# Kernel tuning notes

Measured on AMD Instinct MI355X. Metric: run time of the kernel, lower is better.

Reference implementation:

```python
import jax, jax.numpy as jnp
import numpy as np

B, DIN, DOUT, E = 131072, 512, 512, 16


def setup_inputs() -> dict:
    key = jax.random.key(0)
    k_x, k_wg, k_we = jax.random.split(key, 3)
    x = jax.random.normal(k_x, (B, DIN), dtype=jnp.float32)
    # gating network params
    Wg = jax.random.normal(k_wg, (DIN, E), dtype=jnp.float32) * 0.02
    bg = jnp.zeros((E,), dtype=jnp.float32)
    # GRN params (torch inits them to zero -> GRN is identity at init)
    gamma = jnp.zeros((E,), dtype=jnp.float32)
    beta = jnp.zeros((E,), dtype=jnp.float32)
    # per-expert linear params, stacked [E, DIN, DOUT]
    We = jax.random.normal(k_we, (E, DIN, DOUT), dtype=jnp.float32) * 0.02
    be = jnp.zeros((E, DOUT), dtype=jnp.float32)
    return {"x": x, "Wg": Wg, "bg": bg, "gamma": gamma, "beta": beta,
            "We": We, "be": be, "topk": 2}


def reference(x, Wg, bg, gamma, beta, We, be, topk):
    # ---- gating: linear -> GRN over expert dim -> softmax ----
    logits = x @ Wg + bg                                   # [B, E]
    Gx = jnp.linalg.norm(logits, axis=1, keepdims=True)    # [B, 1] L2 over experts
    Nx = Gx / (jnp.mean(Gx, axis=0, keepdims=True) + 1e-6) # [B, 1]
    logits = gamma * (logits * Nx) + beta + logits         # GRN residual
    gates = jax.nn.softmax(logits, axis=-1)                # [B, E]
    # ---- top-k routing ----
    top_vals, top_idx = jax.lax.top_k(gates, topk)         # [B, k]
    n_tok = x.shape[0]
    # combine weights scattered back to dense [B, E] (zero for unrouted experts)
    w = jnp.zeros_like(gates).at[jnp.arange(n_tok)[:, None], top_idx].add(top_vals)
    # ---- per-expert linear + weighted combine ----
    out = jnp.zeros((n_tok, We.shape[-1]), dtype=x.dtype)
    for e in range(We.shape[0]):  # small fixed loop over experts
        out = out + w[:, e:e + 1] * (x @ We[e] + be[e])
    return out
```

## Files before the change

### kernel.cpp

```cpp
#include <hip/hip_runtime.h>
#include <hip/hip_bf16.h>
#include <stdint.h>

#define NTOK 131072
#define NE 16

typedef __attribute__((ext_vector_type(8))) short short8;
typedef __attribute__((ext_vector_type(4))) float f32x4;

#define AS1 __attribute__((address_space(1)))
#define AS3 __attribute__((address_space(3)))

__device__ __forceinline__ ushort f2bf(float f) {
    __hip_bfloat16 h = __float2bfloat16(f);
    return *reinterpret_cast<ushort*>(&h);
}


__global__ void k_init(int* ctrl) {
    int tid = threadIdx.x;
    if (tid < 144) ctrl[tid] = 0;
}

__global__ __launch_bounds__(256) void k_wet(const float* __restrict__ We, ushort* __restrict__ WeT) {
    __shared__ float t[64][65];
    int e = blockIdx.z, k0 = blockIdx.x * 64, n0 = blockIdx.y * 64;
    int tid = threadIdx.x;
    const float* src = We + ((size_t)e * 512 + k0) * 512 + n0;
    #pragma unroll
    for (int i = 0; i < 16; i++) {
        int idx = i * 256 + tid;
        int r = idx >> 6, c = idx & 63;
        t[r][c] = src[(size_t)r * 512 + c];
    }
    __syncthreads();
    ushort* dst = WeT + ((size_t)e * 512 + n0) * 512 + k0;
    #pragma unroll
    for (int i = 0; i < 16; i++) {
        int idx = i * 256 + tid;
        int rn = idx >> 6, ck = idx & 63;
        dst[(size_t)rn * 512 + ck] = f2bf(t[ck][rn]);
    }
}

__global__ __launch_bounds__(256) void k_gate(const float* __restrict__ x, const float* __restrict__ Wg,
                                              const float* __restrict__ bg, float* __restrict__ logits,
                                              float* __restrict__ partials, ushort* __restrict__ xbf) {
    __shared__ float WgL[512 * 16];
    __shared__ float xs[256][33];
    __shared__ float wsum[4];
    const int tid = threadIdx.x;
    #pragma unroll
    for (int i = 0; i < 32; i++) WgL[i * 256 + tid] = Wg[i * 256 + tid];
    const size_t tokBase = (size_t)blockIdx.x * 256;
    float acc[16];
    #pragma unroll
    for (int e = 0; e < 16; e++) acc[e] = 0.f;

    for (int kc = 0; kc < 16; kc++) {
        __syncthreads();
        #pragma unroll
        for (int i = 0; i < 8; i++) {
            int idx = (i << 8) + tid;
            int rr = idx >> 3, cq = (idx & 7) << 2;
            const float4 v = *(const float4*)&x[(tokBase + rr) * 512 + (kc << 5) + cq];
            xs[rr][cq] = v.x; xs[rr][cq + 1] = v.y; xs[rr][cq + 2] = v.z; xs[rr][cq + 3] = v.w;
            if (xbf) {
                ushort4 uw;
                uw.x = f2bf(v.x); uw.y = f2bf(v.y); uw.z = f2bf(v.z); uw.w = f2bf(v.w);
                *(ushort4*)&xbf[(tokBase + rr) * 512 + (kc << 5) + cq] = uw;
            }
        }
        __syncthreads();
        #pragma unroll
        for (int j = 0; j < 32; j++) {
            float xv = xs[tid][j];
            const float* wr = &WgL[((kc << 5) + j) << 4];
            #pragma unroll
            for (int e = 0; e < 16; e++) acc[e] = fmaf(xv, wr[e], acc[e]);
        }
    }

    float lg[16];
    float ss = 0.f;
    #pragma unroll
    for (int e = 0; e < 16; e++) {
        float v = acc[e] + bg[e];
        lg[e] = v;
        ss += v * v;
    }
    float gx = sqrtf(ss);
    float r = gx;
    #pragma unroll
    for (int off = 32; off >= 1; off >>= 1) r += __shfl_down(r, off);
    if ((tid & 63) == 0) wsum[tid >> 6] = r;
    __syncthreads();
    if (tid == 0) partials[blockIdx.x] = wsum[0] + wsum[1] + wsum[2] + wsum[3];
    float4* lo = (float4*)(logits + (tokBase + tid) * 16);
    lo[0] = make_float4(lg[0], lg[1], lg[2], lg[3]);
    lo[1] = make_float4(lg[4], lg[5], lg[6], lg[7]);
    lo[2] = make_float4(lg[8], lg[9], lg[10], lg[11]);
    lo[3] = make_float4(lg[12], lg[13], lg[14], lg[15]);
}

__global__ void k_redsum(const float* __restrict__ partials, float* __restrict__ sumGx) {
    int tid = threadIdx.x;
    float s = 0.f;
    #pragma unroll
    for (int i = 0; i < 8; i++) s += partials[tid + i * 64];
    #pragma unroll
    for (int off = 32; off >= 1; off >>= 1) s += __shfl_down(s, off);
    if (tid == 0) *sumGx = s;
}

__global__ __launch_bounds__(256) void k_route(const float* __restrict__ logits, const float* __restrict__ gamma,
                                               const float* __restrict__ beta, const float* __restrict__ sumGx,
                                               int* __restrict__ eP, float2* __restrict__ wP,
                                               int* __restrict__ cnts) {
    __shared__ int h[32];
    int tid = threadIdx.x;
    if (tid < 32) h[tid] = 0;
    __syncthreads();
    float mean = sumGx[0] * (1.0f / 131072.0f);
    float inv_mean = 1.0f / (mean + 1e-6f);
    #pragma unroll
    for (int it = 0; it < 4; it++) {
        size_t t = (size_t)blockIdx.x * 1024 + it * 256 + tid;
        const float4* lr = (const float4*)(logits + t * 16);
        float4 a0 = lr[0], a1 = lr[1], a2 = lr[2], a3 = lr[3];
        float lg[16] = {a0.x, a0.y, a0.z, a0.w, a1.x, a1.y, a1.z, a1.w,
                        a2.x, a2.y, a2.z, a2.w, a3.x, a3.y, a3.z, a3.w};
        float ss = 0.f;
        #pragma unroll
        for (int e = 0; e < 16; e++) ss += lg[e] * lg[e];
        float nx = sqrtf(ss) * inv_mean;
        #pragma unroll
        for (int e = 0; e < 16; e++) lg[e] = gamma[e] * (lg[e] * nx) + beta[e] + lg[e];
        int e1 = 0; float v1 = lg[0];
        #pragma unroll
        for (int e = 1; e < 16; e++) if (lg[e] > v1) { v1 = lg[e]; e1 = e; }
        int e2 = -1; float v2 = -3.4e38f;
        #pragma unroll
        for (int e = 0; e < 16; e++) if (e != e1 && lg[e] > v2) { v2 = lg[e]; e2 = e; }
        float s = 0.f;
        #pragma unroll
        for (int e = 0; e < 16; e++) s += expf(lg[e] - v1);
        float w1 = 1.0f / s;
        float w2 = expf(v2 - v1) / s;
        eP[t] = e1 | (e2 << 8);
        wP[t] = make_float2(w1, w2);
        atomicAdd(&h[e1], 1);
        atomicAdd(&h[16 + e2], 1);
    }
    __syncthreads();
    if (tid < 32) atomicAdd(&cnts[tid], h[tid]);
}

__global__ void k_scan(int* ctrl) {
    if (threadIdx.x == 0) {
        int s = 0;
        for (int e = 0; e < 16; e++) { ctrl[64 + e] = s; s += ctrl[e]; }
        s = 0;
        for (int e = 0; e < 16; e++) { ctrl[80 + e] = s; s += ctrl[16 + e]; }
        int t = 0; ctrl[96] = 0;
        for (int e = 0; e < 16; e++) { t += (ctrl[e] + 63) >> 6; ctrl[96 + e + 1] = t; }
        t = 0; ctrl[113] = 0;
        for (int e = 0; e < 16; e++) { t += (ctrl[16 + e] + 63) >> 6; ctrl[113 + e + 1] = t; }
    }
}

__global__ __launch_bounds__(256) void k_scatter(const int* __restrict__ eP, const float2* __restrict__ wP,
                                                 int* __restrict__ ctrl,
                                                 int* __restrict__ listA, float* __restrict__ wA,
                                                 int* __restrict__ listB, float* __restrict__ wB) {
    __shared__ int h[32];
    __shared__ int base[32];
    int tid = threadIdx.x;
    if (tid < 32) h[tid] = 0;
    __syncthreads();
    int ep[4]; float2 w[4]; int r1[4], r2[4];
    #pragma unroll
    for (int i = 0; i < 4; i++) {
        size_t t = (size_t)blockIdx.x * 1024 + i * 256 + tid;
        ep[i] = eP[t];
        w[i] = wP[t];
        r1[i] = atomicAdd(&h[ep[i] & 255], 1);
        r2[i] = atomicAdd(&h[16 + ((ep[i] >> 8) & 255)], 1);
    }
    __syncthreads();
    if (tid < 32) base[tid] = atomicAdd(&ctrl[32 + tid], h[tid]);
    __syncthreads();
    #pragma unroll
    for (int i = 0; i < 4; i++) {
        size_t t = (size_t)blockIdx.x * 1024 + i * 256 + tid;
        int e1 = ep[i] & 255, e2 = (ep[i] >> 8) & 255;
        int i1 = ctrl[64 + e1] + base[e1] + r1[i];
        listA[i1] = (int)t; wA[i1] = w[i].x;
        int i2 = ctrl[80 + e2] + base[16 + e2] + r2[i];
        listB[i2] = (int)t; wB[i2] = w[i].y;
    }
}

template <int ADD, int ABF>
__global__ __launch_bounds__(256, 3) void k_gemm(const float* __restrict__ x, const ushort* __restrict__ xbf,
                                                 const ushort* __restrict__ WeT,
                                                 const float* __restrict__ be,
                                                 const int* __restrict__ list, const float* __restrict__ wlist,
                                                 const int* __restrict__ cnts, const int* __restrict__ offs,
                                                 const int* __restrict__ tileOff,
                                                 float* __restrict__ out) {
    __shared__ ushort lds[20480];
    const int tid = threadIdx.x;
    const int q = (int)gridDim.x >> 3;
    const int bid = ((int)blockIdx.x & 7) * q + ((int)blockIdx.x >> 3);
    const int ry = bid >> 1;
    const int nh = bid & 1;
    if (ry >= tileOff[16]) return;
    int e = 0;
    #pragma unroll
    for (int i = 1; i < 16; i++) if (ry >= tileOff[i]) e = i;
    const int cnt = cnts[e];
    const int off = offs[e];
    const int rowStart = (ry - tileOff[e]) << 6;
    const int n0 = nh << 8;

    const int sRow = tid >> 2, sQ = tid & 3;
    const int gRow = rowStart + sRow;
    const int tokS = (gRow < cnt) ? list[off + gRow] : 0;
    const float* xrowF = x + (size_t)tokS * 512 + sQ * 16;
    const ushort* xrowH = xbf + (size_t)tokS * 512 + sQ * 16;
    const int aswz = (sRow & 7) << 4;
    const int awr0 = 32768 + sRow * 128;

    const char* weB = (const char*)WeT + (size_t)e * 524288 + (size_t)n0 * 1024;

    const int lane = tid & 63;
    const int wid = tid >> 6;
    const int wN = wid << 6;
    const int l16 = lane & 15;
    const int lq = lane >> 4;
    const int mswz = (l16 & 7) << 4;
    const int kbL = lq << 4;

    f32x4 acc[4][4];
    f32x4 zero = {0.f, 0.f, 0.f, 0.f};
    #pragma unroll
    for (int i = 0; i < 4; i++)
        #pragma unroll
        for (int j = 0; j < 4; j++) acc[i][j] = zero;

    auto stageB = [&](int kt) {
        #pragma unroll
        for (int i = 0; i < 8; i++) {
            int D = (tid << 4) + (i << 12);
            int nr = D >> 7, inner = D & 127;
            int sb = inner ^ ((nr & 7) << 4);
            const char* gp = weB + nr * 1024 + kt * 128 + sb;
            __builtin_amdgcn_global_load_lds((const AS1 void*)gp, (AS3 void*)&lds[D >> 1], 16, 0, 0);
        }
    };
    float4 vaF[4];
    short8 vaH[2];
    auto loadA = [&](int kt) {
        if (ABF) {
            const short8* xp = (const short8*)(xrowH + kt * 64);
            vaH[0] = xp[0]; vaH[1] = xp[1];
        } else {
            const float4* xp = (const float4*)(xrowF + kt * 64);
            #pragma unroll
            for (int j = 0; j < 4; j++) vaF[j] = xp[j];
        }
    };
    auto writeA = [&]() {
        #pragma unroll
        for (int h = 0; h < 2; h++) {
            int db = awr0 + (((sQ << 5) + (h << 4)) ^ aswz);
            if (ABF) {
                *(short8*)((char*)lds + db) = vaH[h];
            } else {
                alignas(16) ushort tw[8];
                float4 p = vaF[h * 2], q2 = vaF[h * 2 + 1];
                tw[0] = f2bf(p.x); tw[1] = f2bf(p.y); tw[2] = f2bf(p.z); tw[3] = f2bf(p.w);
                tw[4] = f2bf(q2.x); tw[5] = f2bf(q2.y); tw[6] = f2bf(q2.z); tw[7] = f2bf(q2.w);
                *(short8*)((char*)lds + db) = *(const short8*)tw;
            }
        }
    };
    auto compute = [&]() {
        #pragma unroll
        for (int ks = 0; ks < 2; ks++) {
            const int kb = (ks << 6) + kbL;
            short8 af[4], bfr[4];
            #pragma unroll
            for (int mf = 0; mf < 4; mf++) {
                int m = (mf << 4) + l16;
                af[mf] = *(const short8*)((const char*)lds + 32768 + (m << 7) + (kb ^ mswz));
            }
            #pragma unroll
            for (int nf = 0; nf < 4; nf++) {
                int n = wN + (nf << 4) + l16;
                bfr[nf] = *(const short8*)((const char*)lds + (n << 7) + (kb ^ mswz));
            }
            #pragma unroll
            for (int mf = 0; mf < 4; mf++)
                #pragma unroll
                for (int nf = 0; nf < 4; nf++)
                    acc[mf][nf] = __builtin_amdgcn_mfma_f32_16x16x32_bf16(af[mf], bfr[nf], acc[mf][nf], 0, 0, 0);
        }
    };

    loadA(0);
    #pragma unroll
    for (int kt = 0; kt < 8; kt++) {
        __syncthreads();
        stageB(kt);
        writeA();
        if (kt < 7) loadA(kt + 1);
        __syncthreads();
        compute();
    }

    float bias[4];
    #pragma unroll
    for (int nf = 0; nf < 4; nf++) bias[nf] = be[e * 512 + n0 + wN + (nf << 4) + l16];
    #pragma unroll
    for (int mf = 0; mf < 4; mf++) {
        int rb = rowStart + (mf << 4) + (lq << 2);
        #pragma unroll
        for (int i = 0; i < 4; i++) {
            int r = rb + i;
            if (r < cnt) {
                int tok = list[off + r];
                float wv = wlist[off + r];
                float* orow = out + (size_t)tok * 512 + n0 + wN + l16;
                #pragma unroll
                for (int nf = 0; nf < 4; nf++) {
                    float v = wv * (acc[mf][nf][i] + bias[nf]);
                    float* op = orow + (nf << 4);
                    if (ADD) *op = *op + v; else *op = v;
                }
            }
        }
    }
}

extern "C" void kernel_launch(void* const* d_in, const int* in_sizes, int n_in,
                              void* d_out, int out_size, void* d_ws, size_t ws_size,
                              hipStream_t stream) {
    const float* x = (const float*)d_in[0];
    const float* Wg = (const float*)d_in[1];
    const float* bg = (const float*)d_in[2];
    const float* gamma = (const float*)d_in[3];
    const float* beta = (const float*)d_in[4];
    const float* We = (const float*)d_in[5];
    const float* be = (const float*)d_in[6];
    float* out = (float*)d_out;
    char* ws = (char*)d_ws;

    ushort* WeT = (ushort*)(ws);
    float* logits = (float*)(ws + 8388608);
    int* listA = (int*)(ws + 16777216);
    float* wA = (float*)(ws + 17301504);
    int* listB = (int*)(ws + 17825792);
    float* wB = (float*)(ws + 18350080);
    int* eP = (int*)(ws + 18874368);
    float2* wP = (float2*)(ws + 19398656);
    int* ctrl = (int*)(ws + 20447232);
    float* ctrlF = (float*)ctrl;
    float* partials = (float*)(ws + 16777216);

    const size_t XBF_OFF = 20480000;
    const size_t XBF_BYTES = (size_t)NTOK * 512 * 2;
    bool useBF = (ws_size >= XBF_OFF + XBF_BYTES);
    ushort* xbf = useBF ? (ushort*)(ws + XBF_OFF) : nullptr;

    k_init<<<1, 256, 0, stream>>>(ctrl);
    k_wet<<<dim3(8, 8, 16), 256, 0, stream>>>(We, WeT);
    k_gate<<<512, 256, 0, stream>>>(x, Wg, bg, logits, partials, xbf);
    k_redsum<<<1, 64, 0, stream>>>(partials, ctrlF + 130);
    k_route<<<128, 256, 0, stream>>>(logits, gamma, beta, ctrlF + 130, eP, wP, ctrl);
    k_scan<<<1, 64, 0, stream>>>(ctrl);
    k_scatter<<<128, 256, 0, stream>>>(eP, wP, ctrl, listA, wA, listB, wB);
    if (useBF) {
        k_gemm<0, 1><<<4160, 256, 0, stream>>>(x, xbf, WeT, be, listA, wA, ctrl, ctrl + 64, ctrl + 96, out);
        k_gemm<1, 1><<<4160, 256, 0, stream>>>(x, xbf, WeT, be, listB, wB, ctrl + 16, ctrl + 80, ctrl + 113, out);
    } else {
        k_gemm<0, 0><<<4160, 256, 0, stream>>>(x, xbf, WeT, be, listA, wA, ctrl, ctrl + 64, ctrl + 96, out);
        k_gemm<1, 0><<<4160, 256, 0, stream>>>(x, xbf, WeT, be, listB, wB, ctrl + 16, ctrl + 80, ctrl + 113, out);
    }
}
```

Baseline: 510.3 us.

## Enlarge expert GEMM tile to 256 rows with 1024-thread blocks and LDS double buffering

The expert GEMM tile grows from 64 to 256 token rows, run by 16 waves laid out 4x4 in 1024-thread blocks. Routing tile counts and the grid size are rescaled to match. LDS is double-buffered so the next K-slice of weights and activations is staged while the current one is computed, which halves the barriers per step. This is meant to cut repeated weight loads per token and hide load latency. The cost is that the 128KB LDS footprint allows only one block per CU, and per-expert tail tiles now pad more rows.

```diff
diff --git a/kernel.cpp b/kernel.cpp
--- a/kernel.cpp
+++ b/kernel.cpp
@@ -163,9 +163,9 @@
         s = 0;
         for (int e = 0; e < 16; e++) { ctrl[80 + e] = s; s += ctrl[16 + e]; }
         int t = 0; ctrl[96] = 0;
-        for (int e = 0; e < 16; e++) { t += (ctrl[e] + 63) >> 6; ctrl[96 + e + 1] = t; }
+        for (int e = 0; e < 16; e++) { t += (ctrl[e] + 255) >> 8; ctrl[96 + e + 1] = t; }
         t = 0; ctrl[113] = 0;
-        for (int e = 0; e < 16; e++) { t += (ctrl[16 + e] + 63) >> 6; ctrl[113 + e + 1] = t; }
+        for (int e = 0; e < 16; e++) { t += (ctrl[16 + e] + 255) >> 8; ctrl[113 + e + 1] = t; }
     }
 }
 
@@ -202,14 +202,14 @@
 }
 
 template <int ADD, int ABF>
-__global__ __launch_bounds__(256, 3) void k_gemm(const float* __restrict__ x, const ushort* __restrict__ xbf,
-                                                 const ushort* __restrict__ WeT,
-                                                 const float* __restrict__ be,
-                                                 const int* __restrict__ list, const float* __restrict__ wlist,
-                                                 const int* __restrict__ cnts, const int* __restrict__ offs,
-                                                 const int* __restrict__ tileOff,
-                                                 float* __restrict__ out) {
-    __shared__ ushort lds[20480];
+__global__ __launch_bounds__(1024, 4) void k_gemm(const float* __restrict__ x, const ushort* __restrict__ xbf,
+                                                  const ushort* __restrict__ WeT,
+                                                  const float* __restrict__ be,
+                                                  const int* __restrict__ list, const float* __restrict__ wlist,
+                                                  const int* __restrict__ cnts, const int* __restrict__ offs,
+                                                  const int* __restrict__ tileOff,
+                                                  float* __restrict__ out) {
+    __shared__ ushort lds[65536];
     const int tid = threadIdx.x;
     const int q = (int)gridDim.x >> 3;
     const int bid = ((int)blockIdx.x & 7) * q + ((int)blockIdx.x >> 3);
@@ -221,7 +221,7 @@
     for (int i = 1; i < 16; i++) if (ry >= tileOff[i]) e = i;
     const int cnt = cnts[e];
     const int off = offs[e];
-    const int rowStart = (ry - tileOff[e]) << 6;
+    const int rowStart = (ry - tileOff[e]) << 8;
     const int n0 = nh << 8;
 
     const int sRow = tid >> 2, sQ = tid & 3;
@@ -230,13 +230,14 @@
     const float* xrowF = x + (size_t)tokS * 512 + sQ * 16;
     const ushort* xrowH = xbf + (size_t)tokS * 512 + sQ * 16;
     const int aswz = (sRow & 7) << 4;
-    const int awr0 = 32768 + sRow * 128;
+    const int awr0 = 65536 + sRow * 128;
 
     const char* weB = (const char*)WeT + (size_t)e * 524288 + (size_t)n0 * 1024;
 
     const int lane = tid & 63;
     const int wid = tid >> 6;
-    const int wN = wid << 6;
+    const int wM = (wid >> 2) << 6;
+    const int wN = (wid & 3) << 6;
     const int l16 = lane & 15;
     const int lq = lane >> 4;
     const int mswz = (l16 & 7) << 4;
@@ -249,14 +250,15 @@
         #pragma unroll
         for (int j = 0; j < 4; j++) acc[i][j] = zero;
 
-    auto stageB = [&](int kt) {
-        #pragma unroll
-        for (int i = 0; i < 8; i++) {
-            int D = (tid << 4) + (i << 12);
+    auto stageB = [&](int kt, int buf) {
+        #pragma unroll
+        for (int i = 0; i < 2; i++) {
+            int D = (tid << 4) + (i << 14);
             int nr = D >> 7, inner = D & 127;
             int sb = inner ^ ((nr & 7) << 4);
             const char* gp = weB + nr * 1024 + kt * 128 + sb;
-            __builtin_amdgcn_global_load_lds((const AS1 void*)gp, (AS3 void*)&lds[D >> 1], 16, 0, 0);
+            __builtin_amdgcn_global_load_lds((const AS1 void*)gp,
+                                             (AS3 void*)&lds[(buf * 32768 + D) >> 1], 16, 0, 0);
         }
     };
     float4 vaF[4];
@@ -271,10 +273,10 @@
             for (int j = 0; j < 4; j++) vaF[j] = xp[j];
         }
     };
-    auto writeA = [&]() {
+    auto writeA = [&](int buf) {
         #pragma unroll
         for (int h = 0; h < 2; h++) {
-            int db = awr0 + (((sQ << 5) + (h << 4)) ^ aswz);
+            int db = awr0 + buf * 32768 + (((sQ << 5) + (h << 4)) ^ aswz);
             if (ABF) {
                 *(short8*)((char*)lds + db) = vaH[h];
             } else {
@@ -286,20 +288,20 @@
             }
         }
     };
-    auto compute = [&]() {
+    auto compute = [&](int buf) {
         #pragma unroll
         for (int ks = 0; ks < 2; ks++) {
             const int kb = (ks << 6) + kbL;
             short8 af[4], bfr[4];
             #pragma unroll
             for (int mf = 0; mf < 4; mf++) {
-                int m = (mf << 4) + l16;
-                af[mf] = *(const short8*)((const char*)lds + 32768 + (m << 7) + (kb ^ mswz));
+                int m = wM + (mf << 4) + l16;
+                af[mf] = *(const short8*)((const char*)lds + 65536 + buf * 32768 + (m << 7) + (kb ^ mswz));
             }
             #pragma unroll
             for (int nf = 0; nf < 4; nf++) {
                 int n = wN + (nf << 4) + l16;
-                bfr[nf] = *(const short8*)((const char*)lds + (n << 7) + (kb ^ mswz));
+                bfr[nf] = *(const short8*)((const char*)lds + buf * 32768 + (n << 7) + (kb ^ mswz));
             }
             #pragma unroll
             for (int mf = 0; mf < 4; mf++)
@@ -309,15 +311,21 @@
         }
     };
 
+    stageB(0, 0);
     loadA(0);
+    writeA(0);
+    __syncthreads();
+
     #pragma unroll
     for (int kt = 0; kt < 8; kt++) {
+        const int buf = kt & 1;
+        if (kt < 7) {
+            stageB(kt + 1, buf ^ 1);
+            loadA(kt + 1);
+        }
+        compute(buf);
+        if (kt < 7) writeA(buf ^ 1);
         __syncthreads();
-        stageB(kt);
-        writeA();
-        if (kt < 7) loadA(kt + 1);
-        __syncthreads();
-        compute();
     }
 
     float bias[4];
@@ -325,7 +333,7 @@
     for (int nf = 0; nf < 4; nf++) bias[nf] = be[e * 512 + n0 + wN + (nf << 4) + l16];
     #pragma unroll
     for (int mf = 0; mf < 4; mf++) {
-        int rb = rowStart + (mf << 4) + (lq << 2);
+        int rb = rowStart + wM + (mf << 4) + (lq << 2);
         #pragma unroll
         for (int i = 0; i < 4; i++) {
             int r = rb + i;
@@ -382,10 +390,10 @@
     k_scan<<<1, 64, 0, stream>>>(ctrl);
     k_scatter<<<128, 256, 0, stream>>>(eP, wP, ctrl, listA, wA, listB, wB);
     if (useBF) {
-        k_gemm<0, 1><<<4160, 256, 0, stream>>>(x, xbf, WeT, be, listA, wA, ctrl, ctrl + 64, ctrl + 96, out);
-        k_gemm<1, 1><<<4160, 256, 0, stream>>>(x, xbf, WeT, be, listB, wB, ctrl + 16, ctrl + 80, ctrl + 113, out);
+        k_gemm<0, 1><<<1056, 1024, 0, stream>>>(x, xbf, WeT, be, listA, wA, ctrl, ctrl + 64, ctrl + 96, out);
+        k_gemm<1, 1><<<1056, 1024, 0, stream>>>(x, xbf, WeT, be, listB, wB, ctrl + 16, ctrl + 80, ctrl + 113, out);
     } else {
-        k_gemm<0, 0><<<4160, 256, 0, stream>>>(x, xbf, WeT, be, listA, wA, ctrl, ctrl + 64, ctrl + 96, out);
-        k_gemm<1, 0><<<4160, 256, 0, stream>>>(x, xbf, WeT, be, listB, wB, ctrl + 16, ctrl + 80, ctrl + 113, out);
-    }
-}
+        k_gemm<0, 0><<<1056, 1024, 0, stream>>>(x, xbf, WeT, be, listA, wA, ctrl, ctrl + 64, ctrl + 96, out);
+        k_gemm<1, 0><<<1056, 1024, 0, stream>>>(x, xbf, WeT, be, listB, wB, ctrl + 16, ctrl + 80, ctrl + 113, out);
+    }
+}
```

Measured after the change: 534.5 us. 4.7% more time.

## Pre-swizzle expert weights into MFMA fragment layout and drop LDS staging in GEMM

Applied to the files above, without the earlier changes.

Expert weights are now transposed into a layout that matches the MFMA B-fragment, so each lane loads its 8 bf16 values with one 16-byte global load. The GEMM no longer stages A or B through LDS and has no barriers; every wave loads fragments straight from global memory and double-buffers them across k-steps using setprio. Tiles become 128 rows by 128 columns with a 2x2 wave layout, and occupancy is raised to 4. This removes LDS traffic and sync cost, but relies on L2/L1 for reuse and issues more global loads per wave, since neighbouring waves load the same A and B fragments again.

```diff
diff --git a/kernel.cpp b/kernel.cpp
--- a/kernel.cpp
+++ b/kernel.cpp
@@ -8,9 +8,6 @@
 typedef __attribute__((ext_vector_type(8))) short short8;
 typedef __attribute__((ext_vector_type(4))) float f32x4;
 
-#define AS1 __attribute__((address_space(1)))
-#define AS3 __attribute__((address_space(3)))
-
 __device__ __forceinline__ ushort f2bf(float f) {
     __hip_bfloat16 h = __float2bfloat16(f);
     return *reinterpret_cast<ushort*>(&h);
@@ -22,7 +19,7 @@
     if (tid < 144) ctrl[tid] = 0;
 }
 
-__global__ __launch_bounds__(256) void k_wet(const float* __restrict__ We, ushort* __restrict__ WeT) {
+__global__ __launch_bounds__(256) void k_wet(const float* __restrict__ We, ushort* __restrict__ WeTF) {
     __shared__ float t[64][65];
     int e = blockIdx.z, k0 = blockIdx.x * 64, n0 = blockIdx.y * 64;
     int tid = threadIdx.x;
@@ -34,12 +31,23 @@
         t[r][c] = src[(size_t)r * 512 + c];
     }
     __syncthreads();
-    ushort* dst = WeT + ((size_t)e * 512 + n0) * 512 + k0;
-    #pragma unroll
-    for (int i = 0; i < 16; i++) {
-        int idx = i * 256 + tid;
-        int rn = idx >> 6, ck = idx & 63;
-        dst[(size_t)rn * 512 + ck] = f2bf(t[ck][rn]);
+    #pragma unroll
+    for (int i = 0; i < 2; i++) {
+        int u = i * 256 + tid;
+        int ktl = u >> 8;
+        int ntl = (u >> 6) & 3;
+        int lane = u & 63;
+        int l16 = lane & 15, lq = lane >> 4;
+        alignas(16) ushort tw[8];
+        #pragma unroll
+        for (int j = 0; j < 8; j++) {
+            int kl = ktl * 32 + lq * 8 + j;
+            int nl = ntl * 16 + l16;
+            tw[j] = f2bf(t[kl][nl]);
+        }
+        size_t o = (size_t)e * 262144 + (size_t)((n0 >> 4) + ntl) * 8192
+                 + (size_t)((k0 >> 5) + ktl) * 512 + lane * 8;
+        *(short8*)(WeTF + o) = *(const short8*)tw;
     }
 }
 
@@ -163,9 +171,9 @@
         s = 0;
         for (int e = 0; e < 16; e++) { ctrl[80 + e] = s; s += ctrl[16 + e]; }
         int t = 0; ctrl[96] = 0;
-        for (int e = 0; e < 16; e++) { t += (ctrl[e] + 63) >> 6; ctrl[96 + e + 1] = t; }
+        for (int e = 0; e < 16; e++) { t += (ctrl[e] + 127) >> 7; ctrl[96 + e + 1] = t; }
         t = 0; ctrl[113] = 0;
-        for (int e = 0; e < 16; e++) { t += (ctrl[16 + e] + 63) >> 6; ctrl[113 + e + 1] = t; }
+        for (int e = 0; e < 16; e++) { t += (ctrl[16 + e] + 127) >> 7; ctrl[113 + e + 1] = t; }
     }
 }
 
@@ -202,45 +210,49 @@
 }
 
 template <int ADD, int ABF>
-__global__ __launch_bounds__(256, 3) void k_gemm(const float* __restrict__ x, const ushort* __restrict__ xbf,
-                                                 const ushort* __restrict__ WeT,
+__global__ __launch_bounds__(256, 4) void k_gemm(const float* __restrict__ x, const ushort* __restrict__ xbf,
+                                                 const ushort* __restrict__ WeTF,
                                                  const float* __restrict__ be,
                                                  const int* __restrict__ list, const float* __restrict__ wlist,
                                                  const int* __restrict__ cnts, const int* __restrict__ offs,
                                                  const int* __restrict__ tileOff,
                                                  float* __restrict__ out) {
-    __shared__ ushort lds[20480];
     const int tid = threadIdx.x;
     const int q = (int)gridDim.x >> 3;
     const int bid = ((int)blockIdx.x & 7) * q + ((int)blockIdx.x >> 3);
-    const int ry = bid >> 1;
-    const int nh = bid & 1;
+    const int ry = bid >> 2;
+    const int nq = bid & 3;
     if (ry >= tileOff[16]) return;
     int e = 0;
     #pragma unroll
     for (int i = 1; i < 16; i++) if (ry >= tileOff[i]) e = i;
     const int cnt = cnts[e];
     const int off = offs[e];
-    const int rowStart = (ry - tileOff[e]) << 6;
-    const int n0 = nh << 8;
-
-    const int sRow = tid >> 2, sQ = tid & 3;
-    const int gRow = rowStart + sRow;
-    const int tokS = (gRow < cnt) ? list[off + gRow] : 0;
-    const float* xrowF = x + (size_t)tokS * 512 + sQ * 16;
-    const ushort* xrowH = xbf + (size_t)tokS * 512 + sQ * 16;
-    const int aswz = (sRow & 7) << 4;
-    const int awr0 = 32768 + sRow * 128;
-
-    const char* weB = (const char*)WeT + (size_t)e * 524288 + (size_t)n0 * 1024;
+    const int rowStart = (ry - tileOff[e]) << 7;
+    const int n0 = nq << 7;
 
     const int lane = tid & 63;
     const int wid = tid >> 6;
-    const int wN = wid << 6;
+    const int wM = (wid >> 1) << 6;
+    const int wC = (wid & 1) << 6;
     const int l16 = lane & 15;
     const int lq = lane >> 4;
-    const int mswz = (l16 & 7) << 4;
-    const int kbL = lq << 4;
+
+    const ushort* ap[4];
+    const float* apF[4];
+    #pragma unroll
+    for (int mf = 0; mf < 4; mf++) {
+        int r = rowStart + wM + (mf << 4) + l16;
+        int tok = (r < cnt) ? list[off + r] : 0;
+        if (ABF) ap[mf] = xbf + (size_t)tok * 512 + lq * 8;
+        else     apF[mf] = x + (size_t)tok * 512 + lq * 8;
+    }
+    const ushort* bp[4];
+    #pragma unroll
+    for (int nf = 0; nf < 4; nf++) {
+        int nt = ((n0 + wC) >> 4) + nf;
+        bp[nf] = WeTF + (size_t)e * 262144 + (size_t)nt * 8192 + lane * 8;
+    }
 
     f32x4 acc[4][4];
     f32x4 zero = {0.f, 0.f, 0.f, 0.f};
@@ -249,90 +261,51 @@
         #pragma unroll
         for (int j = 0; j < 4; j++) acc[i][j] = zero;
 
-    auto stageB = [&](int kt) {
-        #pragma unroll
-        for (int i = 0; i < 8; i++) {
-            int D = (tid << 4) + (i << 12);
-            int nr = D >> 7, inner = D & 127;
-            int sb = inner ^ ((nr & 7) << 4);
-            const char* gp = weB + nr * 1024 + kt * 128 + sb;
-            __builtin_amdgcn_global_load_lds((const AS1 void*)gp, (AS3 void*)&lds[D >> 1], 16, 0, 0);
-        }
+    short8 af[4], bf[4];
+    auto loadF = [&](int kt) {
+        #pragma unroll
+        for (int mf = 0; mf < 4; mf++) {
+            if (ABF) {
+                af[mf] = *(const short8*)(ap[mf] + kt * 32);
+            } else {
+                float4 u = *(const float4*)(apF[mf] + kt * 32);
+                float4 v = *(const float4*)(apF[mf] + kt * 32 + 4);
+                alignas(16) ushort tw[8];
+                tw[0] = f2bf(u.x); tw[1] = f2bf(u.y); tw[2] = f2bf(u.z); tw[3] = f2bf(u.w);
+                tw[4] = f2bf(v.x); tw[5] = f2bf(v.y); tw[6] = f2bf(v.z); tw[7] = f2bf(v.w);
+                af[mf] = *(const short8*)tw;
+            }
+        }
+        #pragma unroll
+        for (int nf = 0; nf < 4; nf++) bf[nf] = *(const short8*)(bp[nf] + kt * 512);
     };
-    float4 vaF[4];
-    short8 vaH[2];
-    auto loadA = [&](int kt) {
-        if (ABF) {
-            const short8* xp = (const short8*)(xrowH + kt * 64);
-            vaH[0] = xp[0]; vaH[1] = xp[1];
-        } else {
-            const float4* xp = (const float4*)(xrowF + kt * 64);
+
+    loadF(0);
+    #pragma unroll 2
+    for (int kt = 0; kt < 16; kt++) {
+        __builtin_amdgcn_s_setprio(1);
+        #pragma unroll
+        for (int mf = 0; mf < 4; mf++)
             #pragma unroll
-            for (int j = 0; j < 4; j++) vaF[j] = xp[j];
-        }
-    };
-    auto writeA = [&]() {
-        #pragma unroll
-        for (int h = 0; h < 2; h++) {
-            int db = awr0 + (((sQ << 5) + (h << 4)) ^ aswz);
-            if (ABF) {
-                *(short8*)((char*)lds + db) = vaH[h];
-            } else {
-                alignas(16) ushort tw[8];
-                float4 p = vaF[h * 2], q2 = vaF[h * 2 + 1];
-                tw[0] = f2bf(p.x); tw[1] = f2bf(p.y); tw[2] = f2bf(p.z); tw[3] = f2bf(p.w);
-                tw[4] = f2bf(q2.x); tw[5] = f2bf(q2.y); tw[6] = f2bf(q2.z); tw[7] = f2bf(q2.w);
-                *(short8*)((char*)lds + db) = *(const short8*)tw;
-            }
-        }
-    };
-    auto compute = [&]() {
-        #pragma unroll
-        for (int ks = 0; ks < 2; ks++) {
-            const int kb = (ks << 6) + kbL;
-            short8 af[4], bfr[4];
-            #pragma unroll
-            for (int mf = 0; mf < 4; mf++) {
-                int m = (mf << 4) + l16;
-                af[mf] = *(const short8*)((const char*)lds + 32768 + (m << 7) + (kb ^ mswz));
-            }
-            #pragma unroll
-            for (int nf = 0; nf < 4; nf++) {
-                int n = wN + (nf << 4) + l16;
-                bfr[nf] = *(const short8*)((const char*)lds + (n << 7) + (kb ^ mswz));
-            }
-            #pragma unroll
-            for (int mf = 0; mf < 4; mf++)
-                #pragma unroll
-                for (int nf = 0; nf < 4; nf++)
-                    acc[mf][nf] = __builtin_amdgcn_mfma_f32_16x16x32_bf16(af[mf], bfr[nf], acc[mf][nf], 0, 0, 0);
-        }
-    };
-
-    loadA(0);
-    #pragma unroll
-    for (int kt = 0; kt < 8; kt++) {
-        __syncthreads();
-        stageB(kt);
-        writeA();
-        if (kt < 7) loadA(kt + 1);
-        __syncthreads();
-        compute();
+            for (int nf = 0; nf < 4; nf++)
+                acc[mf][nf] = __builtin_amdgcn_mfma_f32_16x16x32_bf16(af[mf], bf[nf], acc[mf][nf], 0, 0, 0);
+        __builtin_amdgcn_s_setprio(0);
+        if (kt < 15) loadF(kt + 1);
     }
 
     float bias[4];
     #pragma unroll
-    for (int nf = 0; nf < 4; nf++) bias[nf] = be[e * 512 + n0 + wN + (nf << 4) + l16];
+    for (int nf = 0; nf < 4; nf++) bias[nf] = be[e * 512 + n0 + wC + (nf << 4) + l16];
     #pragma unroll
     for (int mf = 0; mf < 4; mf++) {
-        int rb = rowStart + (mf << 4) + (lq << 2);
+        int rb = rowStart + wM + (mf << 4) + (lq << 2);
         #pragma unroll
         for (int i = 0; i < 4; i++) {
             int r = rb + i;
             if (r < cnt) {
                 int tok = list[off + r];
                 float wv = wlist[off + r];
-                float* orow = out + (size_t)tok * 512 + n0 + wN + l16;
+                float* orow = out + (size_t)tok * 512 + n0 + wC + l16;
                 #pragma unroll
                 for (int nf = 0; nf < 4; nf++) {
                     float v = wv * (acc[mf][nf][i] + bias[nf]);
@@ -357,7 +330,7 @@
     float* out = (float*)d_out;
     char* ws = (char*)d_ws;
 
-    ushort* WeT = (ushort*)(ws);
+    ushort* WeTF = (ushort*)(ws);
     float* logits = (float*)(ws + 8388608);
     int* listA = (int*)(ws + 16777216);
     float* wA = (float*)(ws + 17301504);
@@ -375,17 +348,17 @@
     ushort* xbf = useBF ? (ushort*)(ws + XBF_OFF) : nullptr;
 
     k_init<<<1, 256, 0, stream>>>(ctrl);
-    k_wet<<<dim3(8, 8, 16), 256, 0, stream>>>(We, WeT);
+    k_wet<<<dim3(8, 8, 16), 256, 0, stream>>>(We, WeTF);
     k_gate<<<512, 256, 0, stream>>>(x, Wg, bg, logits, partials, xbf);
     k_redsum<<<1, 64, 0, stream>>>(partials, ctrlF + 130);
     k_route<<<128, 256, 0, stream>>>(logits, gamma, beta, ctrlF + 130, eP, wP, ctrl);
     k_scan<<<1, 64, 0, stream>>>(ctrl);
     k_scatter<<<128, 256, 0, stream>>>(eP, wP, ctrl, listA, wA, listB, wB);
     if (useBF) {
-        k_gemm<0, 1><<<4160, 256, 0, stream>>>(x, xbf, WeT, be, listA, wA, ctrl, ctrl + 64, ctrl + 96, out);
-        k_gemm<1, 1><<<4160, 256, 0, stream>>>(x, xbf, WeT, be, listB, wB, ctrl + 16, ctrl + 80, ctrl + 113, out);
+        k_gemm<0, 1><<<4160, 256, 0, stream>>>(x, xbf, WeTF, be, listA, wA, ctrl, ctrl + 64, ctrl + 96, out);
+        k_gemm<1, 1><<<4160, 256, 0, stream>>>(x, xbf, WeTF, be, listB, wB, ctrl + 16, ctrl + 80, ctrl + 113, out);
     } else {
-        k_gemm<0, 0><<<4160, 256, 0, stream>>>(x, xbf, WeT, be, listA, wA, ctrl, ctrl + 64, ctrl + 96, out);
-        k_gemm<1, 0><<<4160, 256, 0, stream>>>(x, xbf, WeT, be, listB, wB, ctrl + 16, ctrl + 80, ctrl + 113, out);
-    }
-}
+        k_gemm<0, 0><<<4160, 256, 0, stream>>>(x, xbf, WeTF, be, listA, wA, ctrl, ctrl + 64, ctrl + 96, out);
+        k_gemm<1, 0><<<4160, 256, 0, stream>>>(x, xbf, WeTF, be, listB, wB, ctrl + 16, ctrl + 80, ctrl + 113, out);
+    }
+}
```

Measured after the change: 672.9 us. +31.9%, slower.

## Make expert scatter order-preserving and coalesce GEMM epilogue through LDS

Applied to the files above, without the earlier changes.

The route kernel now records per-block expert histograms, and the scan kernel turns them into exclusive prefix offsets. The scatter kernel uses wave ballots and those offsets to place tokens in a stable order, replacing LDS and global atomics. Expert token lists therefore stay sorted by token index, so gathered and scattered rows are more regular. The GEMM epilogue stages weighted results in LDS and writes full output rows with float4 stores (read-modify-write for the second pass), adding extra barriers and LDS traffic in exchange for coalesced global accesses.

```diff
diff --git a/kernel.cpp b/kernel.cpp
--- a/kernel.cpp
+++ b/kernel.cpp
@@ -116,7 +116,7 @@
 __global__ __launch_bounds__(256) void k_route(const float* __restrict__ logits, const float* __restrict__ gamma,
                                                const float* __restrict__ beta, const float* __restrict__ sumGx,
                                                int* __restrict__ eP, float2* __restrict__ wP,
-                                               int* __restrict__ cnts) {
+                                               int* __restrict__ cnts, int* __restrict__ blockHist) {
     __shared__ int h[32];
     int tid = threadIdx.x;
     if (tid < 32) h[tid] = 0;
@@ -153,51 +153,76 @@
         atomicAdd(&h[16 + e2], 1);
     }
     __syncthreads();
-    if (tid < 32) atomicAdd(&cnts[tid], h[tid]);
-}
-
-__global__ void k_scan(int* ctrl) {
-    if (threadIdx.x == 0) {
+    if (tid < 32) {
+        atomicAdd(&cnts[tid], h[tid]);
+        blockHist[blockIdx.x * 32 + tid] = h[tid];
+    }
+}
+
+__global__ void k_scan(int* ctrl, int* blockHist) {
+    int t = threadIdx.x;
+    if (t < 32) {
+        int run = 0;
+        for (int b = 0; b < 128; b++) {
+            int v = blockHist[b * 32 + t];
+            blockHist[b * 32 + t] = run;
+            run += v;
+        }
+    }
+    __syncthreads();
+    if (t == 0) {
         int s = 0;
         for (int e = 0; e < 16; e++) { ctrl[64 + e] = s; s += ctrl[e]; }
         s = 0;
         for (int e = 0; e < 16; e++) { ctrl[80 + e] = s; s += ctrl[16 + e]; }
-        int t = 0; ctrl[96] = 0;
-        for (int e = 0; e < 16; e++) { t += (ctrl[e] + 63) >> 6; ctrl[96 + e + 1] = t; }
-        t = 0; ctrl[113] = 0;
-        for (int e = 0; e < 16; e++) { t += (ctrl[16 + e] + 63) >> 6; ctrl[113 + e + 1] = t; }
+        int tt = 0; ctrl[96] = 0;
+        for (int e = 0; e < 16; e++) { tt += (ctrl[e] + 63) >> 6; ctrl[96 + e + 1] = tt; }
+        tt = 0; ctrl[113] = 0;
+        for (int e = 0; e < 16; e++) { tt += (ctrl[16 + e] + 63) >> 6; ctrl[113 + e + 1] = tt; }
     }
 }
 
 __global__ __launch_bounds__(256) void k_scatter(const int* __restrict__ eP, const float2* __restrict__ wP,
-                                                 int* __restrict__ ctrl,
+                                                 const int* __restrict__ ctrl, const int* __restrict__ blockHist,
                                                  int* __restrict__ listA, float* __restrict__ wA,
                                                  int* __restrict__ listB, float* __restrict__ wB) {
-    __shared__ int h[32];
-    __shared__ int base[32];
-    int tid = threadIdx.x;
-    if (tid < 32) h[tid] = 0;
-    __syncthreads();
-    int ep[4]; float2 w[4]; int r1[4], r2[4];
-    #pragma unroll
-    for (int i = 0; i < 4; i++) {
-        size_t t = (size_t)blockIdx.x * 1024 + i * 256 + tid;
-        ep[i] = eP[t];
-        w[i] = wP[t];
-        r1[i] = atomicAdd(&h[ep[i] & 255], 1);
-        r2[i] = atomicAdd(&h[16 + ((ep[i] >> 8) & 255)], 1);
-    }
-    __syncthreads();
-    if (tid < 32) base[tid] = atomicAdd(&ctrl[32 + tid], h[tid]);
-    __syncthreads();
-    #pragma unroll
-    for (int i = 0; i < 4; i++) {
-        size_t t = (size_t)blockIdx.x * 1024 + i * 256 + tid;
-        int e1 = ep[i] & 255, e2 = (ep[i] >> 8) & 255;
-        int i1 = ctrl[64 + e1] + base[e1] + r1[i];
-        listA[i1] = (int)t; wA[i1] = w[i].x;
-        int i2 = ctrl[80 + e2] + base[16 + e2] + r2[i];
-        listB[i2] = (int)t; wB[i2] = w[i].y;
+    __shared__ int waveCnt[4][32];
+    __shared__ int runCnt[32];
+    const int tid = threadIdx.x;
+    const int lane = tid & 63;
+    const int wv = tid >> 6;
+    if (tid < 32) runCnt[tid] = blockHist[blockIdx.x * 32 + tid];
+    __syncthreads();
+    const unsigned long long below = (1ull << lane) - 1ull;
+    for (int it = 0; it < 4; it++) {
+        size_t t = (size_t)blockIdx.x * 1024 + it * 256 + tid;
+        int ep = eP[t];
+        float2 w = wP[t];
+        int e1 = ep & 255, e2 = (ep >> 8) & 255;
+        int r1 = 0, r2 = 0;
+        for (int e = 0; e < 16; e++) {
+            unsigned long long m1 = __ballot(e1 == e);
+            unsigned long long m2 = __ballot(e2 == e);
+            if (e1 == e) r1 = __popcll(m1 & below);
+            if (e2 == e) r2 = __popcll(m2 & below);
+            if (lane == e) {
+                waveCnt[wv][e] = __popcll(m1);
+                waveCnt[wv][16 + e] = __popcll(m2);
+            }
+        }
+        __syncthreads();
+        if (tid < 32) {
+            int s = runCnt[tid];
+            #pragma unroll
+            for (int ww = 0; ww < 4; ww++) { int v = waveCnt[ww][tid]; waveCnt[ww][tid] = s; s += v; }
+            runCnt[tid] = s;
+        }
+        __syncthreads();
+        int i1 = ctrl[64 + e1] + waveCnt[wv][e1] + r1;
+        listA[i1] = (int)t; wA[i1] = w.x;
+        int i2 = ctrl[80 + e2] + waveCnt[wv][16 + e2] + r2;
+        listB[i2] = (int)t; wB[i2] = w.y;
+        __syncthreads();
     }
 }
 
@@ -323,24 +348,40 @@
     float bias[4];
     #pragma unroll
     for (int nf = 0; nf < 4; nf++) bias[nf] = be[e * 512 + n0 + wN + (nf << 4) + l16];
+    float* lsf = (float*)lds;
+    __syncthreads();
     #pragma unroll
     for (int mf = 0; mf < 4; mf++) {
         int rb = rowStart + (mf << 4) + (lq << 2);
         #pragma unroll
         for (int i = 0; i < 4; i++) {
             int r = rb + i;
+            float wv_ = (r < cnt) ? wlist[off + r] : 0.f;
+            int lrow = (lq << 2) + i;
+            #pragma unroll
+            for (int nf = 0; nf < 4; nf++)
+                lsf[lrow * 260 + wN + (nf << 4) + l16] = wv_ * (acc[mf][nf][i] + bias[nf]);
+        }
+        __syncthreads();
+        {
+            int lrow = tid >> 4, seg = tid & 15;
+            int r = rowStart + (mf << 4) + lrow;
             if (r < cnt) {
                 int tok = list[off + r];
-                float wv = wlist[off + r];
-                float* orow = out + (size_t)tok * 512 + n0 + wN + l16;
+                float* orow = out + (size_t)tok * 512 + n0;
                 #pragma unroll
-                for (int nf = 0; nf < 4; nf++) {
-                    float v = wv * (acc[mf][nf][i] + bias[nf]);
-                    float* op = orow + (nf << 4);
-                    if (ADD) *op = *op + v; else *op = v;
+                for (int j = 0; j < 4; j++) {
+                    int c = (seg << 2) + (j << 6);
+                    float4 v = *(float4*)&lsf[lrow * 260 + c];
+                    if (ADD) {
+                        float4 o = *(const float4*)&orow[c];
+                        v.x += o.x; v.y += o.y; v.z += o.z; v.w += o.w;
+                    }
+                    *(float4*)&orow[c] = v;
                 }
             }
         }
+        __syncthreads();
     }
 }
 
@@ -366,6 +407,7 @@
     int* eP = (int*)(ws + 18874368);
     float2* wP = (float2*)(ws + 19398656);
     int* ctrl = (int*)(ws + 20447232);
+    int* blockHist = (int*)(ws + 20451328);
     float* ctrlF = (float*)ctrl;
     float* partials = (float*)(ws + 16777216);
 
@@ -378,9 +420,9 @@
     k_wet<<<dim3(8, 8, 16), 256, 0, stream>>>(We, WeT);
     k_gate<<<512, 256, 0, stream>>>(x, Wg, bg, logits, partials, xbf);
     k_redsum<<<1, 64, 0, stream>>>(partials, ctrlF + 130);
-    k_route<<<128, 256, 0, stream>>>(logits, gamma, beta, ctrlF + 130, eP, wP, ctrl);
-    k_scan<<<1, 64, 0, stream>>>(ctrl);
-    k_scatter<<<128, 256, 0, stream>>>(eP, wP, ctrl, listA, wA, listB, wB);
+    k_route<<<128, 256, 0, stream>>>(logits, gamma, beta, ctrlF + 130, eP, wP, ctrl, blockHist);
+    k_scan<<<1, 64, 0, stream>>>(ctrl, blockHist);
+    k_scatter<<<128, 256, 0, stream>>>(eP, wP, ctrl, blockHist, listA, wA, listB, wB);
     if (useBF) {
         k_gemm<0, 1><<<4160, 256, 0, stream>>>(x, xbf, WeT, be, listA, wA, ctrl, ctrl + 64, ctrl + 96, out);
         k_gemm<1, 1><<<4160, 256, 0, stream>>>(x, xbf, WeT, be, listB, wB, ctrl + 16, ctrl + 80, ctrl + 113, out);
```

After: 481.9 us. 5.6% less time.
